# Optimization experiments

Hardware: AMD Instinct MI355X
Metric: run time of the kernel (lower is better)

## Reference

```python
import jax, jax.numpy as jnp
import numpy as np
from jax import lax

BN_EPS = 1e-5


def fake_quant(x, bits):
    # trax-style symmetric fixed-point fake quant, UPWARD (round-half-up) rounding,
    # range [-1, 1 - 2^-(bits-1)], straight-through estimator for grads.
    s = jnp.asarray(2.0 ** (bits - 1), x.dtype)
    q = jnp.clip(jnp.floor(x * s + 0.5), -s, s - 1.0) / s
    return x + lax.stop_gradient(q - x)


def conv1d(x, w):
    # x: [N, C, L], w: [O, I, K], padding=1, stride=1
    return lax.conv_general_dilated(x, w, window_strides=(1,), padding=((1, 1),),
                                    dimension_numbers=('NCH', 'OIH', 'NCH'))


def setup_inputs() -> dict:
    key = jax.random.key(0)
    ks = jax.random.split(key, 9)
    B, L = 16, 524288
    return {
        'x': jax.random.normal(ks[0], (B, 4, L), jnp.float32),
        'w1': jax.random.normal(ks[1], (8, 4, 3), jnp.float32) * 0.3,
        'b1': jax.random.normal(ks[2], (8,), jnp.float32) * 0.1,
        'gamma': jax.random.uniform(ks[3], (8,), jnp.float32, 0.5, 1.5),
        'beta': jax.random.normal(ks[4], (8,), jnp.float32) * 0.1,
        'bn_mean': jax.random.normal(ks[5], (8,), jnp.float32) * 0.1,
        'bn_var': jax.random.uniform(ks[6], (8,), jnp.float32, 0.5, 1.5),
        'w2': jax.random.normal(ks[7], (2, 8, 3), jnp.float32) * 0.3,
        'b2': jax.random.normal(ks[8], (2,), jnp.float32) * 0.1,
    }


def reference(x, w1, b1, gamma, beta, bn_mean, bn_var, w2, b2):
    BW_F, BW_W, BW_B = 8, 8, 8
    # input fake-quant (activation_post_process)
    x = fake_quant(x, BW_F)
    # ConvBn1d: fold BN into conv weight/bias, fake-quant folded params
    sf = gamma * lax.rsqrt(bn_var + BN_EPS)                    # [8]
    wq = fake_quant(w1 * sf[:, None, None], BW_W)              # [8,4,3]
    bq = fake_quant((b1 - bn_mean) * sf + beta, BW_B)          # [8]
    y = conv1d(x, wq) + bq[None, :, None]                      # [B,8,L]
    y = fake_quant(y, BW_F)
    # Conv1d (quantized weight + bias, no BN, no ReLU since act=False)
    z = conv1d(y, fake_quant(w2, BW_W)) + fake_quant(b2, BW_B)[None, :, None]
    z = fake_quant(z, BW_F)                                    # [B,2,L]
    return z
```

## Files before the change

### kernel.cpp

```cpp
#include <hip/hip_runtime.h>
#include <hip/hip_bf16.h>


#define T 8

__device__ __forceinline__ float fq8(float v) {
    float t = floorf(fmaf(v, 128.0f, 0.5f));
    t = fmaxf(t, -128.0f);
    t = fminf(t, 127.0f);
    return t * 0.0078125f;
}

__global__ __launch_bounds__(256) void fused_qconv_kernel(
    const float* __restrict__ x,
    const float* __restrict__ w1, const float* __restrict__ b1,
    const float* __restrict__ gamma, const float* __restrict__ beta,
    const float* __restrict__ bn_mean, const float* __restrict__ bn_var,
    const float* __restrict__ w2, const float* __restrict__ b2,
    float* __restrict__ out,
    int L, int chunksPerRow, int totalChunks)
{
    __shared__ float s_wq[96];
    __shared__ float s_bq[8];
    __shared__ float s_w2q[48];
    __shared__ float s_b2q[2];

    const int t = threadIdx.x;
    if (t < 96) {
        int c = t / 12;
        float sf = gamma[c] * (1.0f / sqrtf(bn_var[c] + 1e-5f));
        s_wq[t] = fq8(w1[t] * sf);
    } else if (t < 104) {
        int c = t - 96;
        float sf = gamma[c] * (1.0f / sqrtf(bn_var[c] + 1e-5f));
        s_bq[c] = fq8((b1[c] - bn_mean[c]) * sf + beta[c]);
    } else if (t < 152) {
        s_w2q[t - 104] = fq8(w2[t - 104]);
    } else if (t < 154) {
        s_b2q[t - 152] = fq8(b2[t - 152]);
    }
    __syncthreads();

    const int chunk = blockIdx.x * blockDim.x + t;
    if (chunk >= totalChunks) return;
    const int n  = chunk / chunksPerRow;
    const int pc = chunk - n * chunksPerRow;
    const long pos0 = (long)pc * T;
    const bool le = (pos0 == 0);
    const bool re = (pos0 + T == L);

    float xq[4][T + 4];
    const float* xb = x + ((size_t)n * 4) * (size_t)L + pos0;
#pragma unroll
    for (int i = 0; i < 4; ++i) {
        const float* xr = xb + (size_t)i * (size_t)L;
        float4 a = *(const float4*)(xr);
        float4 b = *(const float4*)(xr + 4);
        xq[i][2] = fq8(a.x); xq[i][3] = fq8(a.y); xq[i][4] = fq8(a.z); xq[i][5] = fq8(a.w);
        xq[i][6] = fq8(b.x); xq[i][7] = fq8(b.y); xq[i][8] = fq8(b.z); xq[i][9] = fq8(b.w);
        xq[i][0]      = le ? 0.0f : fq8(xr[-2]);
        xq[i][1]      = le ? 0.0f : fq8(xr[-1]);
        xq[i][T + 2]  = re ? 0.0f : fq8(xr[T]);
        xq[i][T + 3]  = re ? 0.0f : fq8(xr[T + 1]);
    }

    float acc[2][T];
#pragma unroll
    for (int j = 0; j < T; ++j) { acc[0][j] = s_b2q[0]; acc[1][j] = s_b2q[1]; }

#pragma unroll
    for (int c = 0; c < 8; ++c) {
        float wc[12];
#pragma unroll
        for (int q = 0; q < 12; ++q) wc[q] = s_wq[c * 12 + q];
        const float bc  = s_bq[c];
        const float w20 = s_w2q[c * 3 + 0];
        const float w21 = s_w2q[c * 3 + 1];
        const float w22 = s_w2q[c * 3 + 2];
        const float w23 = s_w2q[24 + c * 3 + 0];
        const float w24 = s_w2q[24 + c * 3 + 1];
        const float w25 = s_w2q[24 + c * 3 + 2];

#pragma unroll
        for (int p = 0; p < T + 2; ++p) {
            float v = bc;
#pragma unroll
            for (int i = 0; i < 4; ++i) {
                v = fmaf(xq[i][p + 0], wc[i * 3 + 0], v);
                v = fmaf(xq[i][p + 1], wc[i * 3 + 1], v);
                v = fmaf(xq[i][p + 2], wc[i * 3 + 2], v);
            }
            float yv = fq8(v);
            if (p == 0     && le) yv = 0.0f;
            if (p == T + 1 && re) yv = 0.0f;
            if (p < T) {
                acc[0][p] = fmaf(yv, w20, acc[0][p]);
                acc[1][p] = fmaf(yv, w23, acc[1][p]);
            }
            if (p >= 1 && p - 1 < T) {
                acc[0][p - 1] = fmaf(yv, w21, acc[0][p - 1]);
                acc[1][p - 1] = fmaf(yv, w24, acc[1][p - 1]);
            }
            if (p >= 2) {
                acc[0][p - 2] = fmaf(yv, w22, acc[0][p - 2]);
                acc[1][p - 2] = fmaf(yv, w25, acc[1][p - 2]);
            }
        }
    }

    float* ob = out + ((size_t)n * 2) * (size_t)L + pos0;
#pragma unroll
    for (int o = 0; o < 2; ++o) {
        float4 r0, r1;
        r0.x = fq8(acc[o][0]); r0.y = fq8(acc[o][1]); r0.z = fq8(acc[o][2]); r0.w = fq8(acc[o][3]);
        r1.x = fq8(acc[o][4]); r1.y = fq8(acc[o][5]); r1.z = fq8(acc[o][6]); r1.w = fq8(acc[o][7]);
        *(float4*)(ob + (size_t)o * (size_t)L)     = r0;
        *(float4*)(ob + (size_t)o * (size_t)L + 4) = r1;
    }
}

extern "C" void kernel_launch(void* const* d_in, const int* in_sizes, int n_in,
                              void* d_out, int out_size, void* d_ws, size_t ws_size,
                              hipStream_t stream) {
    const float* x       = (const float*)d_in[0];
    const float* w1      = (const float*)d_in[1];
    const float* b1      = (const float*)d_in[2];
    const float* gamma   = (const float*)d_in[3];
    const float* beta    = (const float*)d_in[4];
    const float* bn_mean = (const float*)d_in[5];
    const float* bn_var  = (const float*)d_in[6];
    const float* w2      = (const float*)d_in[7];
    const float* b2      = (const float*)d_in[8];
    float* out = (float*)d_out;

    const int B = 16;
    const int L = in_sizes[0] / (B * 4);
    const int chunksPerRow = L / T;
    const int totalChunks  = B * chunksPerRow;
    const int block = 256;
    const int grid = (totalChunks + block - 1) / block;

    fused_qconv_kernel<<<grid, block, 0, stream>>>(
        x, w1, b1, gamma, beta, bn_mean, bn_var, w2, b2, out,
        L, chunksPerRow, totalChunks);
}
```

Before: 240.4 us.

## Work in integer-scaled quantized domain and vectorize halo and weight loads

```diff
diff --git a/kernel.cpp b/kernel.cpp
--- a/kernel.cpp
+++ b/kernel.cpp
@@ -4,12 +4,12 @@
 
 #define T 8
 
-__device__ __forceinline__ float fq8(float v) {
+__device__ __forceinline__ float q128(float v) {
     float t = floorf(fmaf(v, 128.0f, 0.5f));
-    t = fmaxf(t, -128.0f);
-    t = fminf(t, 127.0f);
-    return t * 0.0078125f;
+    return fminf(fmaxf(t, -128.0f), 127.0f);
 }
+
+__device__ __forceinline__ float fq8(float v) { return q128(v) * 0.0078125f; }
 
 __global__ __launch_bounds__(256) void fused_qconv_kernel(
     const float* __restrict__ x,
@@ -18,102 +18,121 @@
     const float* __restrict__ bn_mean, const float* __restrict__ bn_var,
     const float* __restrict__ w2, const float* __restrict__ b2,
     float* __restrict__ out,
-    int L, int chunksPerRow, int totalChunks)
+    int L, int chunksPerRow)
 {
-    __shared__ float s_wq[96];
-    __shared__ float s_bq[8];
-    __shared__ float s_w2q[48];
-    __shared__ float s_b2q[2];
+    __shared__ float s_cw[8][20];
+    __shared__ float s_b2[2];
 
     const int t = threadIdx.x;
-    if (t < 96) {
-        int c = t / 12;
-        float sf = gamma[c] * (1.0f / sqrtf(bn_var[c] + 1e-5f));
-        s_wq[t] = fq8(w1[t] * sf);
-    } else if (t < 104) {
-        int c = t - 96;
-        float sf = gamma[c] * (1.0f / sqrtf(bn_var[c] + 1e-5f));
-        s_bq[c] = fq8((b1[c] - bn_mean[c]) * sf + beta[c]);
-    } else if (t < 152) {
-        s_w2q[t - 104] = fq8(w2[t - 104]);
-    } else if (t < 154) {
-        s_b2q[t - 152] = fq8(b2[t - 152]);
+    if (t < 162) {
+        if (t < 160) {
+            const int c = t / 20, j = t - c * 20;
+            float v;
+            if (j < 12) {
+                float sf = gamma[c] * (1.0f / sqrtf(bn_var[c] + 1e-5f));
+                v = fq8(w1[c * 12 + j] * sf);
+            } else if (j == 12) {
+                float sf = gamma[c] * (1.0f / sqrtf(bn_var[c] + 1e-5f));
+                v = fmaf(fq8((b1[c] - bn_mean[c]) * sf + beta[c]), 128.0f, 0.5f);
+            } else if (j < 16) {
+                v = fq8(w2[c * 3 + (j - 13)]);
+            } else if (j < 19) {
+                v = fq8(w2[24 + c * 3 + (j - 16)]);
+            } else {
+                v = 0.0f;
+            }
+            s_cw[c][j] = v;
+        } else {
+            s_b2[t - 160] = fmaf(fq8(b2[t - 160]), 128.0f, 0.5f);
+        }
     }
     __syncthreads();
 
-    const int chunk = blockIdx.x * blockDim.x + t;
-    if (chunk >= totalChunks) return;
-    const int n  = chunk / chunksPerRow;
-    const int pc = chunk - n * chunksPerRow;
-    const long pos0 = (long)pc * T;
+    const int pc = blockIdx.x * blockDim.x + t;
+    if (pc >= chunksPerRow) return;
+    const int n = blockIdx.y;
+    const int pos0 = pc * T;
     const bool le = (pos0 == 0);
     const bool re = (pos0 + T == L);
 
-    float xq[4][T + 4];
-    const float* xb = x + ((size_t)n * 4) * (size_t)L + pos0;
+    float X[4][12];
+    const float* xb = x + (size_t)(n * 4) * (size_t)L + (unsigned)pos0;
 #pragma unroll
     for (int i = 0; i < 4; ++i) {
-        const float* xr = xb + (size_t)i * (size_t)L;
+        const float* xr = xb + (unsigned)(i * L);
         float4 a = *(const float4*)(xr);
         float4 b = *(const float4*)(xr + 4);
-        xq[i][2] = fq8(a.x); xq[i][3] = fq8(a.y); xq[i][4] = fq8(a.z); xq[i][5] = fq8(a.w);
-        xq[i][6] = fq8(b.x); xq[i][7] = fq8(b.y); xq[i][8] = fq8(b.z); xq[i][9] = fq8(b.w);
-        xq[i][0]      = le ? 0.0f : fq8(xr[-2]);
-        xq[i][1]      = le ? 0.0f : fq8(xr[-1]);
-        xq[i][T + 2]  = re ? 0.0f : fq8(xr[T]);
-        xq[i][T + 3]  = re ? 0.0f : fq8(xr[T + 1]);
+        X[i][2] = q128(a.x); X[i][3] = q128(a.y); X[i][4] = q128(a.z); X[i][5] = q128(a.w);
+        X[i][6] = q128(b.x); X[i][7] = q128(b.y); X[i][8] = q128(b.z); X[i][9] = q128(b.w);
+        if (!le) {
+            float4 h = *(const float4*)(xr - 4);
+            X[i][0] = q128(h.z); X[i][1] = q128(h.w);
+        } else { X[i][0] = 0.0f; X[i][1] = 0.0f; }
+        if (!re) {
+            float4 h = *(const float4*)(xr + 8);
+            X[i][10] = q128(h.x); X[i][11] = q128(h.y);
+        } else { X[i][10] = 0.0f; X[i][11] = 0.0f; }
     }
 
     float acc[2][T];
+    {
+        const float a0 = s_b2[0], a1 = s_b2[1];
 #pragma unroll
-    for (int j = 0; j < T; ++j) { acc[0][j] = s_b2q[0]; acc[1][j] = s_b2q[1]; }
+        for (int j = 0; j < T; ++j) { acc[0][j] = a0; acc[1][j] = a1; }
+    }
 
 #pragma unroll
     for (int c = 0; c < 8; ++c) {
-        float wc[12];
-#pragma unroll
-        for (int q = 0; q < 12; ++q) wc[q] = s_wq[c * 12 + q];
-        const float bc  = s_bq[c];
-        const float w20 = s_w2q[c * 3 + 0];
-        const float w21 = s_w2q[c * 3 + 1];
-        const float w22 = s_w2q[c * 3 + 2];
-        const float w23 = s_w2q[24 + c * 3 + 0];
-        const float w24 = s_w2q[24 + c * 3 + 1];
-        const float w25 = s_w2q[24 + c * 3 + 2];
+        const float4 cw0 = *(const float4*)&s_cw[c][0];
+        const float4 cw1 = *(const float4*)&s_cw[c][4];
+        const float4 cw2 = *(const float4*)&s_cw[c][8];
+        const float4 cw3 = *(const float4*)&s_cw[c][12];
+        const float4 cw4 = *(const float4*)&s_cw[c][16];
+        const float w00 = cw0.x, w01 = cw0.y, w02 = cw0.z;
+        const float w10 = cw0.w, w11 = cw1.x, w12 = cw1.y;
+        const float w20 = cw1.z, w21 = cw1.w, w22 = cw2.x;
+        const float w30 = cw2.y, w31 = cw2.z, w32 = cw2.w;
+        const float bc  = cw3.x;
+        const float u0 = cw3.y, u1 = cw3.z, u2 = cw3.w;
+        const float v0 = cw4.x, v1 = cw4.y, v2 = cw4.z;
 
 #pragma unroll
         for (int p = 0; p < T + 2; ++p) {
             float v = bc;
-#pragma unroll
-            for (int i = 0; i < 4; ++i) {
-                v = fmaf(xq[i][p + 0], wc[i * 3 + 0], v);
-                v = fmaf(xq[i][p + 1], wc[i * 3 + 1], v);
-                v = fmaf(xq[i][p + 2], wc[i * 3 + 2], v);
-            }
-            float yv = fq8(v);
-            if (p == 0     && le) yv = 0.0f;
-            if (p == T + 1 && re) yv = 0.0f;
+            v = fmaf(X[0][p], w00, v); v = fmaf(X[0][p + 1], w01, v); v = fmaf(X[0][p + 2], w02, v);
+            v = fmaf(X[1][p], w10, v); v = fmaf(X[1][p + 1], w11, v); v = fmaf(X[1][p + 2], w12, v);
+            v = fmaf(X[2][p], w20, v); v = fmaf(X[2][p + 1], w21, v); v = fmaf(X[2][p + 2], w22, v);
+            v = fmaf(X[3][p], w30, v); v = fmaf(X[3][p + 1], w31, v); v = fmaf(X[3][p + 2], w32, v);
+            float Y = fminf(fmaxf(floorf(v), -128.0f), 127.0f);
+            if (p == 0     && le) Y = 0.0f;
+            if (p == T + 1 && re) Y = 0.0f;
             if (p < T) {
-                acc[0][p] = fmaf(yv, w20, acc[0][p]);
-                acc[1][p] = fmaf(yv, w23, acc[1][p]);
+                acc[0][p] = fmaf(Y, u0, acc[0][p]);
+                acc[1][p] = fmaf(Y, v0, acc[1][p]);
             }
             if (p >= 1 && p - 1 < T) {
-                acc[0][p - 1] = fmaf(yv, w21, acc[0][p - 1]);
-                acc[1][p - 1] = fmaf(yv, w24, acc[1][p - 1]);
+                acc[0][p - 1] = fmaf(Y, u1, acc[0][p - 1]);
+                acc[1][p - 1] = fmaf(Y, v1, acc[1][p - 1]);
             }
             if (p >= 2) {
-                acc[0][p - 2] = fmaf(yv, w22, acc[0][p - 2]);
-                acc[1][p - 2] = fmaf(yv, w25, acc[1][p - 2]);
+                acc[0][p - 2] = fmaf(Y, u2, acc[0][p - 2]);
+                acc[1][p - 2] = fmaf(Y, v2, acc[1][p - 2]);
             }
         }
     }
 
-    float* ob = out + ((size_t)n * 2) * (size_t)L + pos0;
+    float* ob = out + (size_t)(n * 2) * (size_t)L + (unsigned)pos0;
 #pragma unroll
     for (int o = 0; o < 2; ++o) {
         float4 r0, r1;
-        r0.x = fq8(acc[o][0]); r0.y = fq8(acc[o][1]); r0.z = fq8(acc[o][2]); r0.w = fq8(acc[o][3]);
-        r1.x = fq8(acc[o][4]); r1.y = fq8(acc[o][5]); r1.z = fq8(acc[o][6]); r1.w = fq8(acc[o][7]);
+        r0.x = fminf(fmaxf(floorf(acc[o][0]), -128.0f), 127.0f) * 0.0078125f;
+        r0.y = fminf(fmaxf(floorf(acc[o][1]), -128.0f), 127.0f) * 0.0078125f;
+        r0.z = fminf(fmaxf(floorf(acc[o][2]), -128.0f), 127.0f) * 0.0078125f;
+        r0.w = fminf(fmaxf(floorf(acc[o][3]), -128.0f), 127.0f) * 0.0078125f;
+        r1.x = fminf(fmaxf(floorf(acc[o][4]), -128.0f), 127.0f) * 0.0078125f;
+        r1.y = fminf(fmaxf(floorf(acc[o][5]), -128.0f), 127.0f) * 0.0078125f;
+        r1.z = fminf(fmaxf(floorf(acc[o][6]), -128.0f), 127.0f) * 0.0078125f;
+        r1.w = fminf(fmaxf(floorf(acc[o][7]), -128.0f), 127.0f) * 0.0078125f;
         *(float4*)(ob + (size_t)o * (size_t)L)     = r0;
         *(float4*)(ob + (size_t)o * (size_t)L + 4) = r1;
     }
@@ -136,11 +155,10 @@
     const int B = 16;
     const int L = in_sizes[0] / (B * 4);
     const int chunksPerRow = L / T;
-    const int totalChunks  = B * chunksPerRow;
     const int block = 256;
-    const int grid = (totalChunks + block - 1) / block;
+    const int gridX = (chunksPerRow + block - 1) / block;
 
-    fused_qconv_kernel<<<grid, block, 0, stream>>>(
+    fused_qconv_kernel<<<dim3(gridX, B), block, 0, stream>>>(
         x, w1, b1, gamma, beta, bn_mean, bn_var, w2, b2, out,
-        L, chunksPerRow, totalChunks);
+        L, chunksPerRow);
 }
```

Result: no change. 240.8 us (+0.1%).
